# Kernel optimization log

Measured on AMD Instinct MI355X. Metric: run time of the kernel, lower is better.

The kernel has to match this reference:

```python
import jax, jax.numpy as jnp
import numpy as np

H, W = 250, 400
N_RAYS = H * W          # 100000 (one patch)
N_SAMPLES = 1_000_000
P, C, DIM = 50000, 16, 8
STEP_SIZE = 0.005
DENSITY_SHIFT = 0.0
DENSITY_SCALE = min(1.0 / (1.0 - DENSITY_SHIFT), 25.0)


def setup_inputs() -> dict:
    key = jax.random.key(0)
    ks = jax.random.split(key, 12)
    return {
        "trivecs": jax.random.normal(ks[0], (P, C, 3, DIM), dtype=jnp.float32),
        "densities": jax.random.normal(ks[1], (P, C), dtype=jnp.float32),
        "colors": jax.random.normal(ks[2], (P, C, 3), dtype=jnp.float32),
        "local_gweight_s": jax.random.uniform(ks[3], (N_SAMPLES, 3), dtype=jnp.float32),
        "local_gweight_l": jax.random.uniform(ks[4], (N_SAMPLES, 3), dtype=jnp.float32),
        "t_min": jax.random.uniform(ks[5], (N_RAYS,), dtype=jnp.float32),
        "bg": jax.random.uniform(ks[6], (3,), dtype=jnp.float32),
        "local_gindx_s": jax.random.randint(ks[7], (N_SAMPLES, 3), 0, DIM, dtype=jnp.int32),
        "local_gindx_l": jax.random.randint(ks[8], (N_SAMPLES, 3), 0, DIM, dtype=jnp.int32),
        "tensoRF_id": jax.random.randint(ks[9], (N_SAMPLES,), 0, P, dtype=jnp.int32),
        "ray_id": jnp.sort(jax.random.randint(ks[10], (N_SAMPLES,), 0, N_RAYS, dtype=jnp.int32)),
        "step_id": jax.random.randint(ks[11], (N_SAMPLES,), 0, 200, dtype=jnp.int32),
    }


def reference(trivecs, densities, colors, local_gweight_s, local_gweight_l,
              t_min, bg, local_gindx_s, local_gindx_l, tensoRF_id, ray_id, step_id):
    # --- compute_feature: trilinear tensor-decomposition gather ---
    def interp(a):
        vs = trivecs[tensoRF_id, :, a, local_gindx_s[:, a]]  # [N, C]
        vl = trivecs[tensoRF_id, :, a, local_gindx_l[:, a]]  # [N, C]
        return vs * local_gweight_s[:, a:a + 1] + vl * local_gweight_l[:, a:a + 1]

    feature = interp(0) * interp(1) * interp(2)               # [N, C]
    sigma = (feature * densities[tensoRF_id]).sum(axis=1)     # [N]
    color = jnp.einsum('nc,nck->nk', feature, colors[tensoRF_id])  # [N, 3]

    # --- density activation & alpha ---
    density = jax.nn.softplus(sigma - DENSITY_SHIFT * 10.0) * DENSITY_SCALE
    alpha = 1.0 - jnp.exp(-density * STEP_SIZE)               # [N]

    # --- Alphas2Weights: per-ray exclusive transmittance (ray_id sorted) ---
    log_t = -density * STEP_SIZE                              # == log(1 - alpha)
    seg_total = jax.ops.segment_sum(log_t, ray_id, num_segments=N_RAYS)  # [R]
    seg_offset = jnp.concatenate([jnp.zeros((1,), log_t.dtype),
                                  jnp.cumsum(seg_total)[:-1]])           # [R]
    excl = jnp.cumsum(log_t) - log_t - seg_offset[ray_id]     # within-segment excl cumsum
    weights = alpha * jnp.exp(excl)                           # [N]
    bg_weight = jnp.exp(seg_total)                            # [R], prod(1-alpha) per ray

    # --- ray compositing ---
    rgb = jax.nn.sigmoid(color)                               # [N, 3]
    rgb_map = jax.ops.segment_sum(weights[:, None] * rgb, ray_id, num_segments=N_RAYS)
    rgb_map = rgb_map + bg_weight[:, None] * bg[None, :]
    z_val = t_min[ray_id] + step_id.astype(jnp.float32) * STEP_SIZE
    depth_map = jax.ops.segment_sum(weights * z_val, ray_id, num_segments=N_RAYS)
    alpha_map = 1.0 - bg_weight

    rgb_map = rgb_map.T.reshape(3, H, W)
    depth_map = depth_map.reshape(H, W)
    alpha_map = alpha_map.reshape(H, W)
    return rgb_map, depth_map, alpha_map
```

## Files before the change

### kernel.cpp

```cpp
#include <hip/hip_runtime.h>
#include <math.h>

#define HN       250
#define WN       400
#define N_RAYS   (HN * WN)
#define N_SAMP   1000000
#define P_TENSO  50000
#define STEP_SZ  0.005f
#define DENS_SCALE 1.0f
#define NB_SCAN  ((P_TENSO + 1023) / 1024)


#define OFF_SORT    0
#define OFF_RESULTS 32000000
#define OFF_RANK    48000000
#define OFF_CURSOR  52000000
#define OFF_STARTS  52200000
#define OFF_BSUMS   52400000
#define OFF_FLAG    52400512
#define OFF_RSTART  52401024
#define WS_NEED     (52401024 + 400004 + 64)

#define ROW_STRIDE 20
#define TV_F   (24 * ROW_STRIDE)
#define SLAB_F (TV_F + 16 + 48)

__global__ __launch_bounds__(256) void count_bounds_rank(
    const int* __restrict__ tenso_id,
    const int* __restrict__ ray_id,
    int* __restrict__ cursor,
    int* __restrict__ rank,
    int* __restrict__ ray_start)
{
    int n = blockIdx.x * 256 + threadIdx.x;
    if (n >= N_SAMP) return;

    rank[n] = atomicAdd(&cursor[tenso_id[n]], 1);

    int r = ray_id[n];
    int rprev = (n == 0) ? -1 : ray_id[n - 1];
    for (int q = rprev + 1; q <= r; ++q) ray_start[q] = n;
    if (n == N_SAMP - 1) {
        for (int q = r + 1; q <= N_RAYS; ++q) ray_start[q] = N_SAMP;
    }
}

__global__ __launch_bounds__(256) void scan_fused(
    const int* __restrict__ cursor,
    int* __restrict__ starts,
    int* __restrict__ bsums,
    int* __restrict__ flag)
{
    __shared__ int lds[257];
    const int b = blockIdx.x;
    const int t = threadIdx.x;
    const int base = b * 1024 + t * 4;

    int v[4]; int s = 0;
    #pragma unroll
    for (int i = 0; i < 4; ++i) {
        int idx = base + i;
        v[i] = (idx < P_TENSO) ? cursor[idx] : 0;
        s += v[i];
    }
    lds[t] = s;
    __syncthreads();
    for (int d = 1; d < 256; d <<= 1) {
        int x = (t >= d) ? lds[t - d] : 0;
        __syncthreads();
        lds[t] += x;
        __syncthreads();
    }
    if (t == 255) bsums[b] = lds[255];

    __threadfence();
    __syncthreads();
    if (t == 0) {
        atomicAdd(flag, 1);
        while (atomicAdd(flag, 0) < gridDim.x) { }
    }
    __syncthreads();
    __threadfence();

    if (t < 64) {
        int x = (t < b) ? bsums[t] : 0;
        #pragma unroll
        for (int m = 1; m < 64; m <<= 1) x += __shfl_xor(x, m);
        if (t == 0) lds[256] = x;
    }
    __syncthreads();
    const int pre = lds[256];

    int run = pre + ((t > 0) ? lds[t - 1] : 0);
    #pragma unroll
    for (int i = 0; i < 4; ++i) {
        int idx = base + i;
        if (idx < P_TENSO) starts[idx] = run;
        run += v[i];
    }
}

__global__ __launch_bounds__(256) void build_sorted(
    const int*   __restrict__ tenso_id,
    const int*   __restrict__ rank,
    const int*   __restrict__ starts,
    const int*   __restrict__ gis, const int* __restrict__ gil,
    const float* __restrict__ gws, const float* __restrict__ gwl,
    float4* __restrict__ sorted)
{
    int n = blockIdx.x * 256 + threadIdx.x;
    if (n >= N_SAMP) return;

    const int pos = starts[tenso_id[n]] + rank[n];

    unsigned bits = (unsigned)gis[n*3+0] | ((unsigned)gis[n*3+1] << 3) | ((unsigned)gis[n*3+2] << 6)
                  | ((unsigned)gil[n*3+0] << 9) | ((unsigned)gil[n*3+1] << 12) | ((unsigned)gil[n*3+2] << 15);
    float4 A = make_float4(gws[n*3+0], gws[n*3+1], gws[n*3+2], gwl[n*3+0]);
    float4 B = make_float4(gwl[n*3+1], gwl[n*3+2], __uint_as_float(bits),
                           __uint_as_float((unsigned)n));
    sorted[(size_t)pos * 2 + 0] = A;
    sorted[(size_t)pos * 2 + 1] = B;
}

__global__ __launch_bounds__(256) void gather_phase(
    const float* __restrict__ trivecs,
    const float* __restrict__ densities,
    const float* __restrict__ colors,
    const int*   __restrict__ starts,
    const int*   __restrict__ counts,
    const float4* __restrict__ sorted,
    float* __restrict__ results_f)
{
    __shared__ __align__(16) float lds[4 * SLAB_F];
    const int lane = threadIdx.x & 63;
    const int wv   = threadIdx.x >> 6;
    const int t    = blockIdx.x * 4 + wv;
    if (t >= P_TENSO) return;

    const int start = starts[t];
    const int cnt   = counts[t];
    if (cnt == 0) return;

    float* slab = lds + wv * SLAB_F;
    float* dl   = slab + TV_F;
    float* cl   = dl + 16;

    const float* tvg = trivecs + (size_t)t * 384;
    #pragma unroll
    for (int i = 0; i < 6; ++i) {
        int l = lane + i * 64;
        int c = l / 24;
        int rem = l - c * 24;
        slab[rem * ROW_STRIDE + c] = tvg[l];
    }
    if (lane < 16) dl[lane] = densities[(size_t)t * 16 + lane];
    if (lane < 48) {
        int c = lane / 3, k = lane - c * 3;
        cl[k * 16 + c] = colors[(size_t)t * 48 + lane];
    }

    const int g = lane >> 2;
    const int j = lane & 3;

    const float4 dens4 = *(const float4*)(dl + 4 * j);
    const float4 col0  = *(const float4*)(cl + 4 * j);
    const float4 col1  = *(const float4*)(cl + 16 + 4 * j);
    const float4 col2  = *(const float4*)(cl + 32 + 4 * j);

    const int end = start + cnt;
    const int niter = (cnt + 15) >> 4;

    for (int it = 0; it < niter; ++it) {
        const int pos = start + it * 16 + g;
        const bool valid = (pos < end);
        const int cp = valid ? pos : (end - 1);
        const float4 A = sorted[(size_t)cp * 2 + 0];
        const float4 B = sorted[(size_t)cp * 2 + 1];
        const unsigned bits = __float_as_uint(B.z);
        const unsigned n    = __float_as_uint(B.w);

        float4 f;
        {
            const int is = bits & 7, il = (bits >> 9) & 7;
            const float4 vs = *(const float4*)(slab + is * ROW_STRIDE + 4 * j);
            const float4 vl = *(const float4*)(slab + il * ROW_STRIDE + 4 * j);
            f.x = vs.x * A.x + vl.x * A.w;
            f.y = vs.y * A.x + vl.y * A.w;
            f.z = vs.z * A.x + vl.z * A.w;
            f.w = vs.w * A.x + vl.w * A.w;
        }
        {
            const int is = (bits >> 3) & 7, il = (bits >> 12) & 7;
            const float4 vs = *(const float4*)(slab + (8 + is) * ROW_STRIDE + 4 * j);
            const float4 vl = *(const float4*)(slab + (8 + il) * ROW_STRIDE + 4 * j);
            f.x *= vs.x * A.y + vl.x * B.x;
            f.y *= vs.y * A.y + vl.y * B.x;
            f.z *= vs.z * A.y + vl.z * B.x;
            f.w *= vs.w * A.y + vl.w * B.x;
        }
        {
            const int is = (bits >> 6) & 7, il = (bits >> 15) & 7;
            const float4 vs = *(const float4*)(slab + (16 + is) * ROW_STRIDE + 4 * j);
            const float4 vl = *(const float4*)(slab + (16 + il) * ROW_STRIDE + 4 * j);
            f.x *= vs.x * A.z + vl.x * B.y;
            f.y *= vs.y * A.z + vl.y * B.y;
            f.z *= vs.z * A.z + vl.z * B.y;
            f.w *= vs.w * A.z + vl.w * B.y;
        }

        float s0 = f.x * dens4.x + f.y * dens4.y + f.z * dens4.z + f.w * dens4.w;
        float s1 = f.x * col0.x  + f.y * col0.y  + f.z * col0.z  + f.w * col0.w;
        float s2 = f.x * col1.x  + f.y * col1.y  + f.z * col1.z  + f.w * col1.w;
        float s3 = f.x * col2.x  + f.y * col2.y  + f.z * col2.z  + f.w * col2.w;

        s0 += __shfl_xor(s0, 1); s0 += __shfl_xor(s0, 2);
        s1 += __shfl_xor(s1, 1); s1 += __shfl_xor(s1, 2);
        s2 += __shfl_xor(s2, 1); s2 += __shfl_xor(s2, 2);
        s3 += __shfl_xor(s3, 1); s3 += __shfl_xor(s3, 2);

        const float sj = (j == 0) ? s0 : (j == 1) ? s1 : (j == 2) ? s2 : s3;
        float val;
        if (j == 0) {
            float dens = fmaxf(sj, 0.0f) + __logf(1.0f + __expf(-fabsf(sj)));
            val = -(dens * DENS_SCALE) * STEP_SZ;
        } else {
            val = 1.0f / (1.0f + __expf(-sj));
        }
        if (valid) results_f[(size_t)n * 4 + j] = val;
    }
}

__global__ __launch_bounds__(256) void ray_render(
    const float4* __restrict__ results,
    const float*  __restrict__ t_min,
    const float*  __restrict__ bg,
    const int*    __restrict__ ray_start,
    const int*    __restrict__ step_id,
    float* __restrict__ out)
{
    int r = blockIdx.x * 256 + threadIdx.x;
    if (r >= N_RAYS) return;
    const int s = ray_start[r];
    const int e = ray_start[r + 1];
    const float tmin_r = t_min[r];

    float T = 0.0f, aR = 0.0f, aG = 0.0f, aB = 0.0f, aD = 0.0f;
    for (int n = s; n < e; ++n) {
        float4 res = results[n];
        const float lt = res.x;
        const float w = (1.0f - __expf(lt)) * __expf(T);
        T += lt;
        const float z = tmin_r + (float)step_id[n] * STEP_SZ;
        aR += w * res.y;
        aG += w * res.z;
        aB += w * res.w;
        aD += w * z;
    }
    const float bgw = __expf(T);
    out[0 * N_RAYS + r] = aR + bgw * bg[0];
    out[1 * N_RAYS + r] = aG + bgw * bg[1];
    out[2 * N_RAYS + r] = aB + bgw * bg[2];
    out[3 * N_RAYS + r] = aD;
    out[4 * N_RAYS + r] = 1.0f - bgw;
}

__global__ __launch_bounds__(256) void trivec_render_fallback(
    const float* __restrict__ trivecs, const float* __restrict__ densities,
    const float* __restrict__ colors, const float* __restrict__ gws,
    const float* __restrict__ gwl, const float* __restrict__ t_min,
    const float* __restrict__ bg, const int* __restrict__ gis,
    const int* __restrict__ gil, const int* __restrict__ tenso_id,
    const int* __restrict__ ray_id, const int* __restrict__ step_id,
    float* __restrict__ out)
{
    const int lane = threadIdx.x & 63;
    const int r = blockIdx.x * 4 + (threadIdx.x >> 6);
    if (r >= N_RAYS) return;
    const int c = lane & 15;
    const int g = lane >> 4;
    int lo = 0, hi = N_SAMP;
    while (lo < hi) { int mid = (lo + hi) >> 1; if (ray_id[mid] < r) lo = mid + 1; else hi = mid; }
    const int seg_start = lo;
    hi = N_SAMP;
    while (lo < hi) { int mid = (lo + hi) >> 1; if (ray_id[mid] < r + 1) lo = mid + 1; else hi = mid; }
    const int seg_end = lo;
    const float tmin_r = t_min[r];
    float Tlog = 0.0f, accR = 0.0f, accG = 0.0f, accB = 0.0f, accD = 0.0f;
    const int niter = (seg_end - seg_start + 3) >> 2;
    for (int it = 0; it < niter; ++it) {
        const int n = seg_start + it * 4 + g;
        const bool valid = (n < seg_end);
        const int nc = valid ? n : (seg_end - 1);
        const int tid = tenso_id[nc];
        const float* tv = trivecs + (size_t)tid * 384 + c * 24;
        float f = 1.0f;
        #pragma unroll
        for (int a = 0; a < 3; ++a) {
            const int is = gis[nc*3+a], il = gil[nc*3+a];
            const float wS = gws[nc*3+a], wL = gwl[nc*3+a];
            f *= (tv[a*8+is] * wS + tv[a*8+il] * wL);
        }
        const float dns = densities[(size_t)tid * 16 + c];
        const float* colp = colors + ((size_t)tid * 16 + c) * 3;
        float s0 = f*dns, s1 = f*colp[0], s2 = f*colp[1], s3 = f*colp[2];
        #pragma unroll
        for (int m = 1; m < 16; m <<= 1) {
            s0 += __shfl_xor(s0, m); s1 += __shfl_xor(s1, m);
            s2 += __shfl_xor(s2, m); s3 += __shfl_xor(s3, m);
        }
        float dens = fmaxf(s0, 0.0f) + __logf(1.0f + __expf(-fabsf(s0)));
        const float lt = valid ? (-dens * STEP_SZ) : 0.0f;
        const float alpha = 1.0f - __expf(lt);
        const float rr = 1.0f/(1.0f+__expf(-s1)), gg = 1.0f/(1.0f+__expf(-s2)), bb = 1.0f/(1.0f+__expf(-s3));
        const float z = tmin_r + (float)step_id[nc] * STEP_SZ;
        const float lt0 = __shfl(lt,0), lt1 = __shfl(lt,16), lt2 = __shfl(lt,32), lt3 = __shfl(lt,48);
        float excl = Tlog;
        if (g > 0) excl += lt0;
        if (g > 1) excl += lt1;
        if (g > 2) excl += lt2;
        const float w = alpha * __expf(excl);
        Tlog += lt0 + lt1 + lt2 + lt3;
        accR += w*rr; accG += w*gg; accB += w*bb; accD += w*z;
    }
    accR += __shfl_xor(accR,16); accR += __shfl_xor(accR,32);
    accG += __shfl_xor(accG,16); accG += __shfl_xor(accG,32);
    accB += __shfl_xor(accB,16); accB += __shfl_xor(accB,32);
    accD += __shfl_xor(accD,16); accD += __shfl_xor(accD,32);
    const float bgw = __expf(Tlog);
    if (lane == 0) {
        out[0*N_RAYS+r] = accR + bgw*bg[0];
        out[1*N_RAYS+r] = accG + bgw*bg[1];
        out[2*N_RAYS+r] = accB + bgw*bg[2];
        out[3*N_RAYS+r] = accD;
        out[4*N_RAYS+r] = 1.0f - bgw;
    }
}

extern "C" void kernel_launch(void* const* d_in, const int* in_sizes, int n_in,
                              void* d_out, int out_size, void* d_ws, size_t ws_size,
                              hipStream_t stream) {
    const float* trivecs   = (const float*)d_in[0];
    const float* densities = (const float*)d_in[1];
    const float* colors    = (const float*)d_in[2];
    const float* gws       = (const float*)d_in[3];
    const float* gwl       = (const float*)d_in[4];
    const float* t_min     = (const float*)d_in[5];
    const float* bg        = (const float*)d_in[6];
    const int*   gis       = (const int*)d_in[7];
    const int*   gil       = (const int*)d_in[8];
    const int*   tenso_id  = (const int*)d_in[9];
    const int*   ray_id    = (const int*)d_in[10];
    const int*   step_id   = (const int*)d_in[11];
    float* out = (float*)d_out;

    if (ws_size < (size_t)WS_NEED) {
        trivec_render_fallback<<<(N_RAYS + 3) / 4, 256, 0, stream>>>(
            trivecs, densities, colors, gws, gwl, t_min, bg,
            gis, gil, tenso_id, ray_id, step_id, out);
        return;
    }

    char* ws = (char*)d_ws;
    float4* sorted   = (float4*)(ws + OFF_SORT);
    float4* results  = (float4*)(ws + OFF_RESULTS);
    int*    rank     = (int*)(ws + OFF_RANK);
    int*    cursor   = (int*)(ws + OFF_CURSOR);
    int*    starts   = (int*)(ws + OFF_STARTS);
    int*    bsums    = (int*)(ws + OFF_BSUMS);
    int*    flag     = (int*)(ws + OFF_FLAG);
    int*    raystart = (int*)(ws + OFF_RSTART);

    hipMemsetAsync(ws + OFF_CURSOR, 0, (OFF_FLAG + 64) - OFF_CURSOR, stream);

    count_bounds_rank<<<(N_SAMP + 255) / 256, 256, 0, stream>>>(
        tenso_id, ray_id, cursor, rank, raystart);
    scan_fused<<<NB_SCAN, 256, 0, stream>>>(cursor, starts, bsums, flag);
    build_sorted<<<(N_SAMP + 255) / 256, 256, 0, stream>>>(
        tenso_id, rank, starts, gis, gil, gws, gwl, sorted);
    gather_phase<<<(P_TENSO + 3) / 4, 256, 0, stream>>>(
        trivecs, densities, colors, starts, cursor, sorted, (float*)results);
    ray_render<<<(N_RAYS + 255) / 256, 256, 0, stream>>>(
        results, t_min, bg, raystart, step_id, out);
}
```

Baseline: 297.0 us.

## Replace packed sorted sample buffer with index permutation and parallelize ray compositing

Instead of scattering a packed 32-byte record per sample into tensor-sorted order, the pipeline now builds only an int permutation (tensor id and rank packed into one word), and the gather kernel reads indices and weights directly from the original arrays through the permutation, prefetching the next index. This removes a large scatter write and its readback, at the cost of uncoalesced random reads of 12 separate values per sample. Ray rendering now uses 4 lanes per ray, with a shuffle-based product scan of transmittance and cross-lane reductions, to shorten the serial per-ray loop.

```diff
diff --git a/kernel.cpp b/kernel.cpp
--- a/kernel.cpp
+++ b/kernel.cpp
@@ -11,31 +11,33 @@
 #define NB_SCAN  ((P_TENSO + 1023) / 1024)
 
 
-#define OFF_SORT    0
-#define OFF_RESULTS 32000000
-#define OFF_RANK    48000000
-#define OFF_CURSOR  52000000
-#define OFF_STARTS  52200000
-#define OFF_BSUMS   52400000
-#define OFF_FLAG    52400512
-#define OFF_RSTART  52401024
-#define WS_NEED     (52401024 + 400004 + 64)
+#define OFF_RESULTS 0
+#define OFF_PERM    16000000
+#define OFF_RT      20000000
+#define OFF_CURSOR  24000000
+#define OFF_STARTS  24200000
+#define OFF_BSUMS   24400000
+#define OFF_FLAG    24400512
+#define OFF_RSTART  24401024
+#define WS_NEED     (24401024 + 400004 + 64)
 
 #define ROW_STRIDE 20
 #define TV_F   (24 * ROW_STRIDE)
 #define SLAB_F (TV_F + 16 + 48)
 
-__global__ __launch_bounds__(256) void count_bounds_rank(
+__global__ __launch_bounds__(256) void rank_bounds(
     const int* __restrict__ tenso_id,
     const int* __restrict__ ray_id,
     int* __restrict__ cursor,
-    int* __restrict__ rank,
+    int* __restrict__ rt,
     int* __restrict__ ray_start)
 {
     int n = blockIdx.x * 256 + threadIdx.x;
     if (n >= N_SAMP) return;
 
-    rank[n] = atomicAdd(&cursor[tenso_id[n]], 1);
+    const int tid = tenso_id[n];
+    const int rk = atomicAdd(&cursor[tid], 1);
+    rt[n] = (tid << 16) | rk;
 
     int r = ray_id[n];
     int rprev = (n == 0) ? -1 : ray_id[n - 1];
@@ -100,26 +102,16 @@
     }
 }
 
-__global__ __launch_bounds__(256) void build_sorted(
-    const int*   __restrict__ tenso_id,
-    const int*   __restrict__ rank,
-    const int*   __restrict__ starts,
-    const int*   __restrict__ gis, const int* __restrict__ gil,
-    const float* __restrict__ gws, const float* __restrict__ gwl,
-    float4* __restrict__ sorted)
+__global__ __launch_bounds__(256) void finalize_perm(
+    const int* __restrict__ rt,
+    const int* __restrict__ starts,
+    int* __restrict__ perm)
 {
     int n = blockIdx.x * 256 + threadIdx.x;
     if (n >= N_SAMP) return;
-
-    const int pos = starts[tenso_id[n]] + rank[n];
-
-    unsigned bits = (unsigned)gis[n*3+0] | ((unsigned)gis[n*3+1] << 3) | ((unsigned)gis[n*3+2] << 6)
-                  | ((unsigned)gil[n*3+0] << 9) | ((unsigned)gil[n*3+1] << 12) | ((unsigned)gil[n*3+2] << 15);
-    float4 A = make_float4(gws[n*3+0], gws[n*3+1], gws[n*3+2], gwl[n*3+0]);
-    float4 B = make_float4(gwl[n*3+1], gwl[n*3+2], __uint_as_float(bits),
-                           __uint_as_float((unsigned)n));
-    sorted[(size_t)pos * 2 + 0] = A;
-    sorted[(size_t)pos * 2 + 1] = B;
+    const unsigned w = (unsigned)rt[n];
+    int pos = starts[w >> 16] + (int)(w & 0xFFFFu);
+    perm[pos] = n;
 }
 
 __global__ __launch_bounds__(256) void gather_phase(
@@ -128,7 +120,9 @@
     const float* __restrict__ colors,
     const int*   __restrict__ starts,
     const int*   __restrict__ counts,
-    const float4* __restrict__ sorted,
+    const int*   __restrict__ perm,
+    const int*   __restrict__ gis, const int* __restrict__ gil,
+    const float* __restrict__ gws, const float* __restrict__ gwl,
     float* __restrict__ results_f)
 {
     __shared__ __align__(16) float lds[4 * SLAB_F];
@@ -144,6 +138,13 @@
     float* slab = lds + wv * SLAB_F;
     float* dl   = slab + TV_F;
     float* cl   = dl + 16;
+
+    const int g = lane >> 2;
+    const int j = lane & 3;
+    const int end = start + cnt;
+
+    int p = start + g;
+    int n = perm[(p < end) ? p : (end - 1)];
 
     const float* tvg = trivecs + (size_t)t * 384;
     #pragma unroll
@@ -159,53 +160,52 @@
         cl[k * 16 + c] = colors[(size_t)t * 48 + lane];
     }
 
-    const int g = lane >> 2;
-    const int j = lane & 3;
-
     const float4 dens4 = *(const float4*)(dl + 4 * j);
     const float4 col0  = *(const float4*)(cl + 4 * j);
     const float4 col1  = *(const float4*)(cl + 16 + 4 * j);
     const float4 col2  = *(const float4*)(cl + 32 + 4 * j);
 
-    const int end = start + cnt;
     const int niter = (cnt + 15) >> 4;
 
     for (int it = 0; it < niter; ++it) {
-        const int pos = start + it * 16 + g;
-        const bool valid = (pos < end);
-        const int cp = valid ? pos : (end - 1);
-        const float4 A = sorted[(size_t)cp * 2 + 0];
-        const float4 B = sorted[(size_t)cp * 2 + 1];
-        const unsigned bits = __float_as_uint(B.z);
-        const unsigned n    = __float_as_uint(B.w);
+        const bool valid = (p < end);
+        const int sn = n;
+        const int b3 = sn * 3;
+
+        const int   is0 = gis[b3], is1 = gis[b3 + 1], is2 = gis[b3 + 2];
+        const int   il0 = gil[b3], il1 = gil[b3 + 1], il2 = gil[b3 + 2];
+        const float wa0 = gws[b3], wa1 = gws[b3 + 1], wa2 = gws[b3 + 2];
+        const float wb0 = gwl[b3], wb1 = gwl[b3 + 1], wb2 = gwl[b3 + 2];
+
+        if (it + 1 < niter) {
+            p = start + (it + 1) * 16 + g;
+            n = perm[(p < end) ? p : (end - 1)];
+        }
 
         float4 f;
         {
-            const int is = bits & 7, il = (bits >> 9) & 7;
-            const float4 vs = *(const float4*)(slab + is * ROW_STRIDE + 4 * j);
-            const float4 vl = *(const float4*)(slab + il * ROW_STRIDE + 4 * j);
-            f.x = vs.x * A.x + vl.x * A.w;
-            f.y = vs.y * A.x + vl.y * A.w;
-            f.z = vs.z * A.x + vl.z * A.w;
-            f.w = vs.w * A.x + vl.w * A.w;
+            const float4 vs = *(const float4*)(slab + is0 * ROW_STRIDE + 4 * j);
+            const float4 vl = *(const float4*)(slab + il0 * ROW_STRIDE + 4 * j);
+            f.x = vs.x * wa0 + vl.x * wb0;
+            f.y = vs.y * wa0 + vl.y * wb0;
+            f.z = vs.z * wa0 + vl.z * wb0;
+            f.w = vs.w * wa0 + vl.w * wb0;
         }
         {
-            const int is = (bits >> 3) & 7, il = (bits >> 12) & 7;
-            const float4 vs = *(const float4*)(slab + (8 + is) * ROW_STRIDE + 4 * j);
-            const float4 vl = *(const float4*)(slab + (8 + il) * ROW_STRIDE + 4 * j);
-            f.x *= vs.x * A.y + vl.x * B.x;
-            f.y *= vs.y * A.y + vl.y * B.x;
-            f.z *= vs.z * A.y + vl.z * B.x;
-            f.w *= vs.w * A.y + vl.w * B.x;
+            const float4 vs = *(const float4*)(slab + (8 + is1) * ROW_STRIDE + 4 * j);
+            const float4 vl = *(const float4*)(slab + (8 + il1) * ROW_STRIDE + 4 * j);
+            f.x *= vs.x * wa1 + vl.x * wb1;
+            f.y *= vs.y * wa1 + vl.y * wb1;
+            f.z *= vs.z * wa1 + vl.z * wb1;
+            f.w *= vs.w * wa1 + vl.w * wb1;
         }
         {
-            const int is = (bits >> 6) & 7, il = (bits >> 15) & 7;
-            const float4 vs = *(const float4*)(slab + (16 + is) * ROW_STRIDE + 4 * j);
-            const float4 vl = *(const float4*)(slab + (16 + il) * ROW_STRIDE + 4 * j);
-            f.x *= vs.x * A.z + vl.x * B.y;
-            f.y *= vs.y * A.z + vl.y * B.y;
-            f.z *= vs.z * A.z + vl.z * B.y;
-            f.w *= vs.w * A.z + vl.w * B.y;
+            const float4 vs = *(const float4*)(slab + (16 + is2) * ROW_STRIDE + 4 * j);
+            const float4 vl = *(const float4*)(slab + (16 + il2) * ROW_STRIDE + 4 * j);
+            f.x *= vs.x * wa2 + vl.x * wb2;
+            f.y *= vs.y * wa2 + vl.y * wb2;
+            f.z *= vs.z * wa2 + vl.z * wb2;
+            f.w *= vs.w * wa2 + vl.w * wb2;
         }
 
         float s0 = f.x * dens4.x + f.y * dens4.y + f.z * dens4.z + f.w * dens4.w;
@@ -226,7 +226,7 @@
         } else {
             val = 1.0f / (1.0f + __expf(-sj));
         }
-        if (valid) results_f[(size_t)n * 4 + j] = val;
+        if (valid) results_f[(size_t)sn * 4 + j] = val;
     }
 }
 
@@ -238,30 +238,50 @@
     const int*    __restrict__ step_id,
     float* __restrict__ out)
 {
-    int r = blockIdx.x * 256 + threadIdx.x;
+    const int lane = threadIdx.x & 63;
+    const int g    = lane & 3;
+    const int r    = (blockIdx.x * 256 + threadIdx.x) >> 2;
     if (r >= N_RAYS) return;
     const int s = ray_start[r];
     const int e = ray_start[r + 1];
     const float tmin_r = t_min[r];
 
-    float T = 0.0f, aR = 0.0f, aG = 0.0f, aB = 0.0f, aD = 0.0f;
-    for (int n = s; n < e; ++n) {
-        float4 res = results[n];
-        const float lt = res.x;
-        const float w = (1.0f - __expf(lt)) * __expf(T);
-        T += lt;
-        const float z = tmin_r + (float)step_id[n] * STEP_SZ;
+    float eT = 1.0f, aR = 0.0f, aG = 0.0f, aB = 0.0f, aD = 0.0f;
+    const int niter = (e - s + 3) >> 2;
+    for (int it = 0; it < niter; ++it) {
+        const int idx = s + it * 4 + g;
+        const bool valid = (idx < e);
+        const int ci = valid ? idx : (e - 1);
+        const float4 res = results[ci];
+        const float z = tmin_r + (float)step_id[ci] * STEP_SZ;
+        const float elt = valid ? __expf(res.x) : 1.0f;
+
+        float excl = 1.0f;
+        const float v1 = __shfl_up(elt, 1, 4); if (g >= 1) excl *= v1;
+        const float v2 = __shfl_up(elt, 2, 4); if (g >= 2) excl *= v2;
+        const float v3 = __shfl_up(elt, 3, 4); if (g >= 3) excl *= v3;
+
+        const float w = eT * excl * (1.0f - elt);
         aR += w * res.y;
         aG += w * res.z;
         aB += w * res.w;
         aD += w * z;
-    }
-    const float bgw = __expf(T);
-    out[0 * N_RAYS + r] = aR + bgw * bg[0];
-    out[1 * N_RAYS + r] = aG + bgw * bg[1];
-    out[2 * N_RAYS + r] = aB + bgw * bg[2];
-    out[3 * N_RAYS + r] = aD;
-    out[4 * N_RAYS + r] = 1.0f - bgw;
+
+        const float tot = __shfl(excl * elt, 3, 4);
+        eT *= tot;
+    }
+
+    aR += __shfl_xor(aR, 1); aR += __shfl_xor(aR, 2);
+    aG += __shfl_xor(aG, 1); aG += __shfl_xor(aG, 2);
+    aB += __shfl_xor(aB, 1); aB += __shfl_xor(aB, 2);
+    aD += __shfl_xor(aD, 1); aD += __shfl_xor(aD, 2);
+
+    const float outv = (g == 0) ? aR + eT * bg[0]
+                     : (g == 1) ? aG + eT * bg[1]
+                     : (g == 2) ? aB + eT * bg[2]
+                     : aD;
+    out[g * N_RAYS + r] = outv;
+    if (g == 0) out[4 * N_RAYS + r] = 1.0f - eT;
 }
 
 __global__ __launch_bounds__(256) void trivec_render_fallback(
@@ -361,9 +381,9 @@
     }
 
     char* ws = (char*)d_ws;
-    float4* sorted   = (float4*)(ws + OFF_SORT);
     float4* results  = (float4*)(ws + OFF_RESULTS);
-    int*    rank     = (int*)(ws + OFF_RANK);
+    int*    perm     = (int*)(ws + OFF_PERM);
+    int*    rt       = (int*)(ws + OFF_RT);
     int*    cursor   = (int*)(ws + OFF_CURSOR);
     int*    starts   = (int*)(ws + OFF_STARTS);
     int*    bsums    = (int*)(ws + OFF_BSUMS);
@@ -372,13 +392,14 @@
 
     hipMemsetAsync(ws + OFF_CURSOR, 0, (OFF_FLAG + 64) - OFF_CURSOR, stream);
 
-    count_bounds_rank<<<(N_SAMP + 255) / 256, 256, 0, stream>>>(
-        tenso_id, ray_id, cursor, rank, raystart);
+    rank_bounds<<<(N_SAMP + 255) / 256, 256, 0, stream>>>(
+        tenso_id, ray_id, cursor, rt, raystart);
     scan_fused<<<NB_SCAN, 256, 0, stream>>>(cursor, starts, bsums, flag);
-    build_sorted<<<(N_SAMP + 255) / 256, 256, 0, stream>>>(
-        tenso_id, rank, starts, gis, gil, gws, gwl, sorted);
+    finalize_perm<<<(N_SAMP + 255) / 256, 256, 0, stream>>>(
+        rt, starts, perm);
     gather_phase<<<(P_TENSO + 3) / 4, 256, 0, stream>>>(
-        trivecs, densities, colors, starts, cursor, sorted, (float*)results);
-    ray_render<<<(N_RAYS + 255) / 256, 256, 0, stream>>>(
+        trivecs, densities, colors, starts, cursor, perm,
+        gis, gil, gws, gwl, (float*)results);
+    ray_render<<<(N_RAYS * 4 + 255) / 256, 256, 0, stream>>>(
         results, t_min, bg, raystart, step_id, out);
 }
```

After: 317.0 us. 1.07x slower.
